# Kernel tuning notes

Measured on AMD Instinct MI355X. Metric: run time of the kernel, lower is better.

The kernel has to match this reference:

```python
import jax, jax.numpy as jnp
import numpy as np

N = 50000      # nodes
E = 800000     # edges
G = 512        # graphs
IN = 544; HID = 64; H = 4; OUT = 2
EPS = 1e-5

def setup_inputs():
    key = jax.random.key(0)
    ks = jax.random.split(key, 16)
    x = jax.random.normal(ks[0], (N, IN), jnp.float32)
    edge_index = jax.random.randint(ks[1], (2, E), 0, N, jnp.int64)
    batch = jnp.sort(jax.random.randint(ks[2], (N,), 0, G, jnp.int64))
    s = lambda k, shp, fan: jax.random.normal(k, shp, jnp.float32) / np.sqrt(fan)
    return {
        'x': x, 'edge_index': edge_index, 'batch': batch,
        'ln_g': jnp.ones((32,), jnp.float32), 'ln_b': jnp.zeros((32,), jnp.float32),
        'bn1_g': jnp.ones((512,), jnp.float32), 'bn1_b': jnp.zeros((512,), jnp.float32),
        'Wc': s(ks[3], (16, 512), 512), 'bc': jnp.zeros((16,), jnp.float32),
        'bn2_g': jnp.ones((48,), jnp.float32), 'bn2_b': jnp.zeros((48,), jnp.float32),
        'Wp': s(ks[4], (HID, 48), 48), 'bp': jnp.zeros((HID,), jnp.float32),
        'Wg': s(ks[5], (H * HID, HID), HID),
        'att_src': s(ks[6], (H, HID), HID), 'att_dst': s(ks[7], (H, HID), HID),
        'bg': jnp.zeros((H * HID,), jnp.float32),
        'bn3_g': jnp.ones((H * HID,), jnp.float32), 'bn3_b': jnp.zeros((H * HID,), jnp.float32),
        'W1': s(ks[8], (HID, H * HID), H * HID), 'b1': jnp.zeros((HID,), jnp.float32),
        'W2': s(ks[9], (OUT, HID), HID), 'b2': jnp.zeros((OUT,), jnp.float32),
    }

def _batchnorm(x, g, b):
    mu = jnp.mean(x, axis=0)
    var = jnp.var(x, axis=0)
    return (x - mu) * jax.lax.rsqrt(var + EPS) * g + b

def _forward(x, ln_g, ln_b, bn1_g, bn1_b, Wc, bc, bn2_g, bn2_b, Wp, bp,
             Wg, att_src, att_dst, bg, bn3_g, bn3_b, W1, b1, W2, b2,
             edge_index, batch):
    # feature split + norms
    x_cnn = _batchnorm(x[:, :512], bn1_g, bn1_b)
    f = x[:, 512:]
    mu = jnp.mean(f, axis=-1, keepdims=True)
    var = jnp.var(f, axis=-1, keepdims=True)
    f = (f - mu) * jax.lax.rsqrt(var + EPS) * ln_g + ln_b
    x_cnn = x_cnn @ Wc.T + bc                      # [N,16]
    z = jnp.concatenate([x_cnn, f], axis=1)        # [N,48]
    z = _batchnorm(z, bn2_g, bn2_b)
    z = jax.nn.relu(z @ Wp.T + bp)                 # [N,HID] (dropout=eval identity)
    # GATConv (concat=True, negative_slope=0.2)
    h = (z @ Wg.T).reshape(N, H, HID)              # [N,H,C]
    a_src = jnp.sum(h * att_src, axis=-1)          # [N,H]
    a_dst = jnp.sum(h * att_dst, axis=-1)          # [N,H]
    src, dst = edge_index[0], edge_index[1]
    e = jax.nn.leaky_relu(a_src[src] + a_dst[dst], 0.2)   # [E,H]
    m = jax.ops.segment_max(e, dst, num_segments=N)
    m = jnp.where(jnp.isfinite(m), m, 0.0)
    ex = jnp.exp(e - m[dst])
    s = jax.ops.segment_sum(ex, dst, num_segments=N)
    alpha = ex / jnp.maximum(s, 1e-16)[dst]               # [E,H]
    out = jax.ops.segment_sum(alpha[:, :, None] * h[src], dst, num_segments=N)
    out = out.reshape(N, H * HID) + bg
    # BatchNorm + ELU + mean pool + MLP head
    out = jax.nn.elu(_batchnorm(out, bn3_g, bn3_b))
    cnt = jax.ops.segment_sum(jnp.ones((N,), out.dtype), batch, num_segments=G)
    pooled = jax.ops.segment_sum(out, batch, num_segments=G) / jnp.maximum(cnt, 1.0)[:, None]
    hmlp = jax.nn.relu(pooled @ W1.T + b1)
    return hmlp @ W2.T + b2                        # [G,OUT]

def reference(x, edge_index, batch, ln_g, ln_b, bn1_g, bn1_b, Wc, bc, bn2_g, bn2_b,
              Wp, bp, Wg, att_src, att_dst, bg, bn3_g, bn3_b, W1, b1, W2, b2):
    return _forward(x, ln_g, ln_b, bn1_g, bn1_b, Wc, bc, bn2_g, bn2_b, Wp, bp,
                    Wg, att_src, att_dst, bg, bn3_g, bn3_b, W1, b1, W2, b2,
                    edge_index, batch)
```

## Files before the change

### kernel.cpp

```cpp
#include <hip/hip_runtime.h>

static constexpr int N_   = 50000;
static constexpr int E_   = 800000;
static constexpr int G_   = 512;
static constexpr int IN_  = 544;
static constexpr float EPS_ = 1e-5f;

static constexpr size_t OFF_BN1SUM = 0;
static constexpr size_t OFF_BN1SQ  = 2048;
static constexpr size_t OFF_BN2SUM = 4096;
static constexpr size_t OFF_BN2SQ  = 4288;
static constexpr size_t OFF_BN3SUM = 4480;
static constexpr size_t OFF_BN3SQ  = 5504;
static constexpr size_t OFF_COUNT  = 6528;
static constexpr size_t OFF_CUR    = 206528;
static constexpr size_t ZERO_BYTES = 406528;
static constexpr size_t OFF_OFFS   = 406528;
static constexpr size_t OFF_PART   = 606592;
static constexpr size_t OFF_WC2    = 606848;
static constexpr size_t OFF_C2     = 639616;
static constexpr size_t OFF_WP2    = 639744;
static constexpr size_t OFF_CP     = 652032;
static constexpr size_t OFF_WGT    = 652288;
static constexpr size_t OFF_ASRC   = 719872;
static constexpr size_t OFF_ADST   = 1519872;
static constexpr size_t OFF_SRCS   = 2319872;
static constexpr size_t OFF_Z      = 5519872;
static constexpr size_t OFF_H      = 15119872;
static constexpr size_t OFF_OUTP   = 66319872;
static constexpr size_t OFF_POOL   = 117519872;

#define DEV static __device__ __forceinline__

DEV float lrelu(float v) { return v > 0.f ? v : 0.2f * v; }
DEV unsigned short f2bf(float f) {
    unsigned u = __float_as_uint(f);
    return (unsigned short)((u + 0x7fffu + ((u >> 16) & 1u)) >> 16);
}

__global__ __launch_bounds__(512) void k_bn1_hist(
        const float* __restrict__ x, float* __restrict__ sum, float* __restrict__ sq,
        const int* __restrict__ ei, int* __restrict__ count) {
    __shared__ float4 ta[512];
    __shared__ float4 tb[512];
    int bid = blockIdx.x;
    int t = threadIdx.x;
    if (bid >= 256) {
        int k = (bid - 256) * 512 + t;
        if (k < E_) atomicAdd(&count[ei[E_ + k]], 1);
        return;
    }
    int cq = t & 127, rsub = t >> 7;
    int c4 = cq << 2;
    float4 a = make_float4(0.f, 0.f, 0.f, 0.f);
    float4 b = make_float4(0.f, 0.f, 0.f, 0.f);
    for (int r = bid * 4 + rsub; r < N_; r += 256 * 4) {
        float4 v = *(const float4*)(x + (size_t)r * IN_ + c4);
        a.x += v.x; a.y += v.y; a.z += v.z; a.w += v.w;
        b.x += v.x * v.x; b.y += v.y * v.y; b.z += v.z * v.z; b.w += v.w * v.w;
    }
    ta[t] = a; tb[t] = b;
    __syncthreads();
    if (t < 128) {
        float4 sa = ta[t], sb = tb[t];
#pragma unroll
        for (int r = 1; r < 4; r++) {
            float4 xa = ta[r * 128 + t], xb = tb[r * 128 + t];
            sa.x += xa.x; sa.y += xa.y; sa.z += xa.z; sa.w += xa.w;
            sb.x += xb.x; sb.y += xb.y; sb.z += xb.z; sb.w += xb.w;
        }
        int c = t << 2;
        atomicAdd(&sum[c + 0], sa.x); atomicAdd(&sum[c + 1], sa.y);
        atomicAdd(&sum[c + 2], sa.z); atomicAdd(&sum[c + 3], sa.w);
        atomicAdd(&sq[c + 0], sb.x);  atomicAdd(&sq[c + 1], sb.y);
        atomicAdd(&sq[c + 2], sb.z);  atomicAdd(&sq[c + 3], sb.w);
    }
}

__global__ __launch_bounds__(512) void k_fold1(
        const float* __restrict__ sum, const float* __restrict__ sq,
        const float* __restrict__ g, const float* __restrict__ b,
        const float* __restrict__ Wc, const float* __restrict__ bc,
        float* __restrict__ Wc2t, float* __restrict__ c2) {
    __shared__ float c2s[16];
    int j = threadIdx.x;
    if (j < 16) c2s[j] = 0.f;
    float mu  = sum[j] / (float)N_;
    float var = sq[j] / (float)N_ - mu * mu;
    float s   = g[j] * rsqrtf(var + EPS_);
    float tj  = b[j] - mu * s;
    __syncthreads();
    for (int i = 0; i < 16; i++) {
        float wv = Wc[i * 512 + j];
        Wc2t[i * 512 + j] = wv * s;
        float p = tj * wv;
        for (int m = 1; m < 64; m <<= 1) p += __shfl_xor(p, m);
        if ((j & 63) == 0) atomicAdd(&c2s[i], p);
    }
    __syncthreads();
    if (j < 16) c2[j] = c2s[j] + bc[j];
}

static constexpr int WSTRIDE = 516;
__global__ __launch_bounds__(512) void k_z(
        const float* __restrict__ x, const float* __restrict__ Wc2tg,
        const float* __restrict__ c2g, const float* __restrict__ lng,
        const float* __restrict__ lnb, float* __restrict__ z,
        float* __restrict__ bn2sum, float* __restrict__ bn2sq) {
    __shared__ float wc2[16 * WSTRIDE];
    __shared__ float c2s[16];
    __shared__ float bsum[48];
    __shared__ float bsq[48];
    int t = threadIdx.x;
    for (int q = t; q < 8192; q += 512) {
        int row = q >> 9, col = q & 511;
        wc2[row * WSTRIDE + col] = Wc2tg[q];
    }
    if (t < 16) c2s[t] = c2g[t];
    if (t < 48) { bsum[t] = 0.f; bsq[t] = 0.f; }
    __syncthreads();
    int nd = t >> 3, i = t & 7;
    int node = blockIdx.x * 64 + nd;
    bool valid = node < N_;
    int rn = valid ? node : N_ - 1;
    const float4* xr = (const float4*)(x + (size_t)rn * IN_);
    const float4* w0 = (const float4*)(wc2 + i * WSTRIDE);
    const float4* w1 = (const float4*)(wc2 + (i + 8) * WSTRIDE);
    float acc0 = c2s[i], acc1 = c2s[i + 8];
    for (int u = 0; u < 128; u++) {
        float4 xv = xr[u];
        float4 a4 = w0[u];
        float4 b4 = w1[u];
        acc0 += xv.x * a4.x + xv.y * a4.y + xv.z * a4.z + xv.w * a4.w;
        acc1 += xv.x * b4.x + xv.y * b4.y + xv.z * b4.z + xv.w * b4.w;
    }
    float v[4]; float sm = 0.f, sqv = 0.f;
#pragma unroll
    for (int jj = 0; jj < 4; jj++) {
        v[jj] = x[(size_t)rn * IN_ + 512 + i + 8 * jj];
        sm += v[jj]; sqv += v[jj] * v[jj];
    }
    for (int m = 1; m < 8; m <<= 1) {
        sm  += __shfl_xor(sm, m);
        sqv += __shfl_xor(sqv, m);
    }
    float mu  = sm * (1.f / 32.f);
    float var = sqv * (1.f / 32.f) - mu * mu;
    float rs  = rsqrtf(var + EPS_);
    float outc[6];
    outc[0] = acc0; outc[1] = acc1;
#pragma unroll
    for (int jj = 0; jj < 4; jj++) {
        int c = i + 8 * jj;
        outc[2 + jj] = (v[jj] - mu) * rs * lng[c] + lnb[c];
    }
    if (valid) {
        z[node * 48 + i]     = acc0;
        z[node * 48 + i + 8] = acc1;
#pragma unroll
        for (int jj = 0; jj < 4; jj++) z[node * 48 + 16 + i + 8 * jj] = outc[2 + jj];
    }
    float s6[6], q6[6];
#pragma unroll
    for (int k = 0; k < 6; k++) {
        float vv = valid ? outc[k] : 0.f;
        s6[k] = vv; q6[k] = vv * vv;
    }
#pragma unroll
    for (int m = 8; m < 64; m <<= 1) {
#pragma unroll
        for (int k = 0; k < 6; k++) {
            s6[k] += __shfl_xor(s6[k], m);
            q6[k] += __shfl_xor(q6[k], m);
        }
    }
    if ((t & 63) < 8) {
        int cols[6] = { i, i + 8, 16 + i, 24 + i, 32 + i, 40 + i };
#pragma unroll
        for (int k = 0; k < 6; k++) {
            atomicAdd(&bsum[cols[k]], s6[k]);
            atomicAdd(&bsq[cols[k]],  q6[k]);
        }
    }
    __syncthreads();
    if (t < 48) {
        atomicAdd(&bn2sum[t], bsum[t]);
        atomicAdd(&bn2sq[t],  bsq[t]);
    }
}

__global__ __launch_bounds__(256) void k_fold2_wgt(
        const float* __restrict__ sum, const float* __restrict__ sq,
        const float* __restrict__ g, const float* __restrict__ b,
        const float* __restrict__ Wp, const float* __restrict__ bp,
        float* __restrict__ Wp2, float* __restrict__ cp,
        const float* __restrict__ Wg, float* __restrict__ Wgt) {
    __shared__ float t2[48];
    int t = threadIdx.x;
    if (blockIdx.x > 0) {
        int idx = (blockIdx.x - 1) * 256 + t;
        int c = idx >> 6, k = idx & 63;
        Wgt[k * 256 + c] = Wg[idx];
        return;
    }
    if (t < 48) {
        float mu  = sum[t] / (float)N_;
        float var = sq[t] / (float)N_ - mu * mu;
        float s   = g[t] * rsqrtf(var + EPS_);
        t2[t] = b[t] - mu * s;
        for (int k = 0; k < 64; k++) Wp2[t * 64 + k] = Wp[k * 48 + t] * s;
    }
    __syncthreads();
    if (t < 64) {
        float acc = bp[t];
        for (int j = 0; j < 48; j++) acc += t2[j] * Wp[t * 48 + j];
        cp[t] = acc;
    }
}

__global__ void k_scan1(const int* __restrict__ count, int* __restrict__ offs,
                        int* __restrict__ part) {
    __shared__ int sd[1024];
    int t = threadIdx.x;
    int idx = blockIdx.x * 1024 + t;
    int v = (idx < N_) ? count[idx] : 0;
    sd[t] = v;
    for (int off = 1; off < 1024; off <<= 1) {
        __syncthreads();
        int tmp = (t >= off) ? sd[t - off] : 0;
        __syncthreads();
        sd[t] += tmp;
    }
    if (idx < N_) offs[idx] = sd[t] - v;
    if (t == 1023) part[blockIdx.x] = sd[1023];
}
__global__ void k_scan23(int* __restrict__ offs, const int* __restrict__ part) {
    __shared__ int bs;
    int t = threadIdx.x, b = blockIdx.x;
    if (t < 64) {
        int v = (t < b) ? part[t] : 0;
        for (int m = 1; m < 64; m <<= 1) v += __shfl_xor(v, m);
        if (t == 0) bs = v;
    }
    __syncthreads();
    int idx = b * 1024 + t;
    if (idx < N_) offs[idx] += bs;
}

__global__ void k_scatter(const int* __restrict__ ei, const int* __restrict__ offs,
                          int* __restrict__ cur, int* __restrict__ srcsort) {
    int k = blockIdx.x * 256 + threadIdx.x;
    int src = ei[k], dst = ei[E_ + k];
    int pos = offs[dst] + atomicAdd(&cur[dst], 1);
    srcsort[pos] = src;
}

__global__ __launch_bounds__(512) void k_h2(
        const float* __restrict__ z, const float* __restrict__ Wp2g,
        const float* __restrict__ cpg, const float* __restrict__ Wgtg,
        const float* __restrict__ att_s, const float* __restrict__ att_d,
        ushort4* __restrict__ hbf, float* __restrict__ asrc, float* __restrict__ adst) {
    __shared__ float4 wgh[32 * 64];
    __shared__ float  z1t[128 * 64];
    __shared__ float  wp2[48 * 64];
    __shared__ float  cps[64];
    __shared__ float4 ats[64];
    __shared__ float4 atd[64];
    int t = threadIdx.x;
    int base = blockIdx.x * 128;
    {
        const float4* z4 = (const float4*)(z + (size_t)base * 48);
        float4* zt4 = (float4*)wgh;
        for (int q = t; q < 1536; q += 512) zt4[q] = z4[q];
    }
    for (int q = t; q < 3072; q += 512) wp2[q] = Wp2g[q];
    if (t < 64) {
        cps[t] = cpg[t];
        ats[t] = ((const float4*)att_s)[t];
        atd[t] = ((const float4*)att_d)[t];
    }
    __syncthreads();
    int w = t >> 6, l = t & 63;
    {
        float wpr[48];
#pragma unroll
        for (int j = 0; j < 48; j++) wpr[j] = wp2[j * 64 + l];
        const float* zt = (const float*)wgh;
        for (int p = 0; p < 16; p++) {
            int nd = p * 8 + w;
            float acc = cps[l];
            const float* zr = zt + nd * 48;
#pragma unroll
            for (int j = 0; j < 48; j++) acc += zr[j] * wpr[j];
            z1t[nd * 64 + l] = fmaxf(acc, 0.f);
        }
    }
    const float4* wg4 = (const float4*)Wgtg;
    float4 acc[16];
#pragma unroll
    for (int nd = 0; nd < 16; nd++) acc[nd] = make_float4(0.f, 0.f, 0.f, 0.f);
    for (int half = 0; half < 2; half++) {
        __syncthreads();
        for (int q = t; q < 2048; q += 512) wgh[q] = wg4[half * 2048 + q];
        __syncthreads();
        int kbase = half * 32;
        for (int kk = 0; kk < 32; kk++) {
            float4 wv = wgh[kk * 64 + l];
            int k = kbase + kk;
#pragma unroll
            for (int nd = 0; nd < 16; nd++) {
                float zv = z1t[(w * 16 + nd) * 64 + k];
                acc[nd].x += zv * wv.x; acc[nd].y += zv * wv.y;
                acc[nd].z += zv * wv.z; acc[nd].w += zv * wv.w;
            }
        }
    }
    float4 as4 = ats[l], ad4 = atd[l];
#pragma unroll
    for (int nd = 0; nd < 16; nd++) {
        int node = base + w * 16 + nd;
        if (node < N_) {
            ushort4 hv;
            hv.x = f2bf(acc[nd].x); hv.y = f2bf(acc[nd].y);
            hv.z = f2bf(acc[nd].z); hv.w = f2bf(acc[nd].w);
            hbf[(size_t)node * 64 + l] = hv;
            float pa = acc[nd].x * as4.x + acc[nd].y * as4.y +
                       acc[nd].z * as4.z + acc[nd].w * as4.w;
            float pb = acc[nd].x * ad4.x + acc[nd].y * ad4.y +
                       acc[nd].z * ad4.z + acc[nd].w * ad4.w;
            for (int m = 1; m < 16; m <<= 1) {
                pa += __shfl_xor(pa, m);
                pb += __shfl_xor(pb, m);
            }
            if ((l & 15) == 0) {
                asrc[node * 4 + (l >> 4)] = pa;
                adst[node * 4 + (l >> 4)] = pb;
            }
        }
    }
}

__global__ __launch_bounds__(256) void k_agg(
        const int* __restrict__ count, const int* __restrict__ offs,
        const int* __restrict__ srcsort, const float* __restrict__ asrc,
        const float* __restrict__ adst, const ushort4* __restrict__ hbf,
        const float* __restrict__ bg, float* __restrict__ outpre) {
    __shared__ int   s_src[4][128];
    __shared__ float s_wf[4][512];
    int w = threadIdx.x >> 6, l = threadIdx.x & 63;
    int dst = blockIdx.x * 4 + w;
    const float4* asrc4 = (const float4*)asrc;
    float4* out4 = (float4*)outpre;
    float4 bgv = ((const float4*)bg)[l];
    int deg = count[dst];
    if (deg == 0) { out4[dst * 64 + l] = bgv; return; }
    int base = offs[dst];
    float4 ad = ((const float4*)adst)[dst];
    const float NEGINF = -__builtin_inff();
    float4 e0 = make_float4(NEGINF, NEGINF, NEGINF, NEGINF);
    float4 e1 = make_float4(NEGINF, NEGINF, NEGINF, NEGINF);
    if (l < deg) {
        int s0 = srcsort[base + l];
        s_src[w][l] = s0;
        float4 a = asrc4[s0];
        e0 = make_float4(lrelu(a.x + ad.x), lrelu(a.y + ad.y),
                         lrelu(a.z + ad.z), lrelu(a.w + ad.w));
    }
    if (l + 64 < deg) {
        int s1 = srcsort[base + l + 64];
        s_src[w][l + 64] = s1;
        float4 a = asrc4[s1];
        e1 = make_float4(lrelu(a.x + ad.x), lrelu(a.y + ad.y),
                         lrelu(a.z + ad.z), lrelu(a.w + ad.w));
    }
    float4 mx = make_float4(fmaxf(e0.x, e1.x), fmaxf(e0.y, e1.y),
                            fmaxf(e0.z, e1.z), fmaxf(e0.w, e1.w));
    for (int j = l + 128; j < deg; j += 64) {
        int s2 = srcsort[base + j];
        float4 a = asrc4[s2];
        mx.x = fmaxf(mx.x, lrelu(a.x + ad.x)); mx.y = fmaxf(mx.y, lrelu(a.y + ad.y));
        mx.z = fmaxf(mx.z, lrelu(a.z + ad.z)); mx.w = fmaxf(mx.w, lrelu(a.w + ad.w));
    }
    for (int m = 1; m < 64; m <<= 1) {
        mx.x = fmaxf(mx.x, __shfl_xor(mx.x, m));
        mx.y = fmaxf(mx.y, __shfl_xor(mx.y, m));
        mx.z = fmaxf(mx.z, __shfl_xor(mx.z, m));
        mx.w = fmaxf(mx.w, __shfl_xor(mx.w, m));
    }
    float4 sv = make_float4(0.f, 0.f, 0.f, 0.f);
    if (l < deg) {
        float4 ex = make_float4(__expf(e0.x - mx.x), __expf(e0.y - mx.y),
                                __expf(e0.z - mx.z), __expf(e0.w - mx.w));
        *(float4*)&s_wf[w][l * 4] = ex;
        sv.x += ex.x; sv.y += ex.y; sv.z += ex.z; sv.w += ex.w;
    }
    if (l + 64 < deg) {
        float4 ex = make_float4(__expf(e1.x - mx.x), __expf(e1.y - mx.y),
                                __expf(e1.z - mx.z), __expf(e1.w - mx.w));
        *(float4*)&s_wf[w][(l + 64) * 4] = ex;
        sv.x += ex.x; sv.y += ex.y; sv.z += ex.z; sv.w += ex.w;
    }
    for (int j = l + 128; j < deg; j += 64) {
        int s2 = srcsort[base + j];
        float4 a = asrc4[s2];
        sv.x += __expf(lrelu(a.x + ad.x) - mx.x);
        sv.y += __expf(lrelu(a.y + ad.y) - mx.y);
        sv.z += __expf(lrelu(a.z + ad.z) - mx.z);
        sv.w += __expf(lrelu(a.w + ad.w) - mx.w);
    }
    for (int m = 1; m < 64; m <<= 1) {
        sv.x += __shfl_xor(sv.x, m); sv.y += __shfl_xor(sv.y, m);
        sv.z += __shfl_xor(sv.z, m); sv.w += __shfl_xor(sv.w, m);
    }
    int hd = l >> 4;
    float mh  = hd == 0 ? mx.x : hd == 1 ? mx.y : hd == 2 ? mx.z : mx.w;
    float sh  = hd == 0 ? sv.x : hd == 1 ? sv.y : hd == 2 ? sv.z : sv.w;
    float adh = hd == 0 ? ad.x : hd == 1 ? ad.y : hd == 2 ? ad.z : ad.w;
    float inv = 1.f / fmaxf(sh, 1e-16f);
    float4 accv = make_float4(0.f, 0.f, 0.f, 0.f);
    const uint2* h2p = (const uint2*)hbf;
    int dcap = deg < 128 ? deg : 128;
#pragma unroll 2
    for (int j = 0; j < dcap; j++) {
        int src = s_src[w][j];
        float wgt = s_wf[w][j * 4 + hd] * inv;
        uint2 u = h2p[(size_t)src * 64 + l];
        accv.x += wgt * __uint_as_float(u.x << 16);
        accv.y += wgt * __uint_as_float(u.x & 0xffff0000u);
        accv.z += wgt * __uint_as_float(u.y << 16);
        accv.w += wgt * __uint_as_float(u.y & 0xffff0000u);
    }
    for (int j = 128; j < deg; j++) {
        int src = srcsort[base + j];
        float4 a = asrc4[src];
        float ah = hd == 0 ? a.x : hd == 1 ? a.y : hd == 2 ? a.z : a.w;
        float wgt = __expf(lrelu(ah + adh) - mh) * inv;
        uint2 u = h2p[(size_t)src * 64 + l];
        accv.x += wgt * __uint_as_float(u.x << 16);
        accv.y += wgt * __uint_as_float(u.x & 0xffff0000u);
        accv.z += wgt * __uint_as_float(u.y << 16);
        accv.w += wgt * __uint_as_float(u.y & 0xffff0000u);
    }
    out4[dst * 64 + l] = make_float4(accv.x + bgv.x, accv.y + bgv.y,
                                     accv.z + bgv.z, accv.w + bgv.w);
}

__global__ __launch_bounds__(256) void k_bn3_stats(
        const float* __restrict__ op, float* __restrict__ sum, float* __restrict__ sq) {
    __shared__ float4 ta[256];
    __shared__ float4 tb[256];
    int t = threadIdx.x;
    int cq = t & 63, rsub = t >> 6;
    int c4 = cq << 2;
    float4 a = make_float4(0.f, 0.f, 0.f, 0.f);
    float4 b = make_float4(0.f, 0.f, 0.f, 0.f);
    for (int r = blockIdx.x * 4 + rsub; r < N_; r += gridDim.x * 4) {
        float4 v = *(const float4*)(op + (size_t)r * 256 + c4);
        a.x += v.x; a.y += v.y; a.z += v.z; a.w += v.w;
        b.x += v.x * v.x; b.y += v.y * v.y; b.z += v.z * v.z; b.w += v.w * v.w;
    }
    ta[t] = a; tb[t] = b;
    __syncthreads();
    if (t < 64) {
        float4 sa = ta[t], sb = tb[t];
#pragma unroll
        for (int r = 1; r < 4; r++) {
            float4 xa = ta[r * 64 + t], xb = tb[r * 64 + t];
            sa.x += xa.x; sa.y += xa.y; sa.z += xa.z; sa.w += xa.w;
            sb.x += xb.x; sb.y += xb.y; sb.z += xb.z; sb.w += xb.w;
        }
        int c = t << 2;
        atomicAdd(&sum[c + 0], sa.x); atomicAdd(&sum[c + 1], sa.y);
        atomicAdd(&sum[c + 2], sa.z); atomicAdd(&sum[c + 3], sa.w);
        atomicAdd(&sq[c + 0], sb.x);  atomicAdd(&sq[c + 1], sb.y);
        atomicAdd(&sq[c + 2], sb.z);  atomicAdd(&sq[c + 3], sb.w);
    }
}

__global__ __launch_bounds__(256) void k_pool_mlp(
        const float* __restrict__ op, const int* __restrict__ batch,
        const float* __restrict__ bn3sum, const float* __restrict__ bn3sq,
        const float* __restrict__ bn3g, const float* __restrict__ bn3b,
        const float* __restrict__ W1, const float* __restrict__ b1,
        const float* __restrict__ W2, const float* __restrict__ b2,
        float* __restrict__ out) {
    __shared__ float4 tile[256];
    __shared__ float  pl[256];
    __shared__ float  hm[64];
    int g = blockIdx.x;
    int t = threadIdx.x;
    int cq = t & 63, rsub = t >> 6;
    int c4 = cq << 2;
    int lo = 0, hi = N_;
    while (lo < hi) { int mid = (lo + hi) >> 1; if (batch[mid] < g) lo = mid + 1; else hi = mid; }
    int start = lo;
    hi = N_;
    while (lo < hi) { int mid = (lo + hi) >> 1; if (batch[mid] < g + 1) lo = mid + 1; else hi = mid; }
    int end = lo;
    float scv[4], shv[4];
#pragma unroll
    for (int k = 0; k < 4; k++) {
        int c = c4 + k;
        float mu  = bn3sum[c] / (float)N_;
        float var = bn3sq[c] / (float)N_ - mu * mu;
        float s   = bn3g[c] * rsqrtf(var + EPS_);
        scv[k] = s; shv[k] = bn3b[c] - mu * s;
    }
    float4 acc = make_float4(0.f, 0.f, 0.f, 0.f);
    for (int n = start + rsub; n < end; n += 4) {
        float4 v = *(const float4*)(op + (size_t)n * 256 + c4);
        float e0 = v.x * scv[0] + shv[0], e1 = v.y * scv[1] + shv[1];
        float e2 = v.z * scv[2] + shv[2], e3 = v.w * scv[3] + shv[3];
        acc.x += (e0 > 0.f) ? e0 : expm1f(e0);
        acc.y += (e1 > 0.f) ? e1 : expm1f(e1);
        acc.z += (e2 > 0.f) ? e2 : expm1f(e2);
        acc.w += (e3 > 0.f) ? e3 : expm1f(e3);
    }
    tile[t] = acc;
    __syncthreads();
    if (t < 64) {
        float4 s = tile[t];
#pragma unroll
        for (int r = 1; r < 4; r++) {
            float4 xv = tile[r * 64 + t];
            s.x += xv.x; s.y += xv.y; s.z += xv.z; s.w += xv.w;
        }
        float icn = 1.f / fmaxf((float)(end - start), 1.f);
        ((float4*)pl)[t] = make_float4(s.x * icn, s.y * icn, s.z * icn, s.w * icn);
    }
    __syncthreads();
    {
        int j = t >> 2, part = t & 3;
        const float* w1r = W1 + j * 256 + part * 64;
        const float* plr = pl + part * 64;
        float a = 0.f;
#pragma unroll
        for (int c = 0; c < 64; c++) a += w1r[c] * plr[c];
        a += __shfl_xor(a, 1);
        a += __shfl_xor(a, 2);
        if (part == 0) hm[j] = fmaxf(a + b1[j], 0.f);
    }
    __syncthreads();
    if (t < 128) {
        int j = t >> 6, k = t & 63;
        float p = W2[j * 64 + k] * hm[k];
        for (int m = 1; m < 64; m <<= 1) p += __shfl_xor(p, m);
        if (k == 0) out[g * 2 + j] = p + b2[j];
    }
}

extern "C" void kernel_launch(void* const* d_in, const int* in_sizes, int n_in,
                              void* d_out, int out_size, void* d_ws, size_t ws_size,
                              hipStream_t stream) {
    const float* x    = (const float*)d_in[0];
    const int*   ei   = (const int*)d_in[1];
    const int*   batch= (const int*)d_in[2];
    const float* lng  = (const float*)d_in[3];
    const float* lnb  = (const float*)d_in[4];
    const float* bn1g = (const float*)d_in[5];
    const float* bn1b = (const float*)d_in[6];
    const float* Wc   = (const float*)d_in[7];
    const float* bc   = (const float*)d_in[8];
    const float* bn2g = (const float*)d_in[9];
    const float* bn2b = (const float*)d_in[10];
    const float* Wp   = (const float*)d_in[11];
    const float* bp   = (const float*)d_in[12];
    const float* Wg   = (const float*)d_in[13];
    const float* atts = (const float*)d_in[14];
    const float* attd = (const float*)d_in[15];
    const float* bg   = (const float*)d_in[16];
    const float* bn3g = (const float*)d_in[17];
    const float* bn3b = (const float*)d_in[18];
    const float* W1   = (const float*)d_in[19];
    const float* b1   = (const float*)d_in[20];
    const float* W2   = (const float*)d_in[21];
    const float* b2   = (const float*)d_in[22];
    float* out = (float*)d_out;

    char* w8 = (char*)d_ws;
    float* bn1sum = (float*)(w8 + OFF_BN1SUM);
    float* bn1sq  = (float*)(w8 + OFF_BN1SQ);
    float* bn2sum = (float*)(w8 + OFF_BN2SUM);
    float* bn2sq  = (float*)(w8 + OFF_BN2SQ);
    float* bn3sum = (float*)(w8 + OFF_BN3SUM);
    float* bn3sq  = (float*)(w8 + OFF_BN3SQ);
    int*   count  = (int*)(w8 + OFF_COUNT);
    int*   cur    = (int*)(w8 + OFF_CUR);
    int*   offs   = (int*)(w8 + OFF_OFFS);
    int*   part   = (int*)(w8 + OFF_PART);
    float* Wc2t   = (float*)(w8 + OFF_WC2);
    float* c2     = (float*)(w8 + OFF_C2);
    float* Wp2    = (float*)(w8 + OFF_WP2);
    float* cp     = (float*)(w8 + OFF_CP);
    float* Wgt    = (float*)(w8 + OFF_WGT);
    float* asrc   = (float*)(w8 + OFF_ASRC);
    float* adst   = (float*)(w8 + OFF_ADST);
    int*   srcs   = (int*)(w8 + OFF_SRCS);
    float* z      = (float*)(w8 + OFF_Z);
    ushort4* hbf  = (ushort4*)(w8 + OFF_H);
    float* outp   = (float*)(w8 + OFF_OUTP);

    hipMemsetAsync(d_ws, 0, ZERO_BYTES, stream);

    const int HISTB = (E_ + 511) / 512;
    k_bn1_hist<<<256 + HISTB, 512, 0, stream>>>(x, bn1sum, bn1sq, ei, count);
    k_fold1<<<1, 512, 0, stream>>>(bn1sum, bn1sq, bn1g, bn1b, Wc, bc, Wc2t, c2);
    k_z<<<(N_ + 63) / 64, 512, 0, stream>>>(x, Wc2t, c2, lng, lnb, z, bn2sum, bn2sq);
    const int SCANB = (N_ + 1023) / 1024;
    k_scan1<<<SCANB, 1024, 0, stream>>>(count, offs, part);
    k_scan23<<<SCANB, 1024, 0, stream>>>(offs, part);
    k_fold2_wgt<<<65, 256, 0, stream>>>(bn2sum, bn2sq, bn2g, bn2b, Wp, bp, Wp2, cp, Wg, Wgt);
    k_scatter<<<E_ / 256, 256, 0, stream>>>(ei, offs, cur, srcs);
    k_h2<<<(N_ + 127) / 128, 512, 0, stream>>>(z, Wp2, cp, Wgt, atts, attd, hbf, asrc, adst);
    k_agg<<<N_ / 4, 256, 0, stream>>>(count, offs, srcs, asrc, adst, hbf, bg, outp);
    k_bn3_stats<<<256, 256, 0, stream>>>(outp, bn3sum, bn3sq);
    k_pool_mlp<<<G_, 256, 0, stream>>>(outp, batch, bn3sum, bn3sq, bn3g, bn3b,
                                       W1, b1, W2, b2, out);
}
```

Measured before the change: 555.0 us.

## Store GAT output in bf16, tile k_z over node pairs, vectorize k_h2 loops

The aggregation output is now stored as bf16 instead of fp32, which halves the bytes written by k_agg and read by the bn3 stats and pooling kernels. The edge histogram is merged into the grid-stride loop of the bn1 stats kernel, which now runs with a fixed 2048x256 grid. k_z computes two nodes per thread so each weight read from shared memory is reused, and k_h2 uses float4 loads from shared memory in both of its inner products. k_bn3_stats also gets more blocks. Rounding to bf16 adds error to the BN3 statistics and to the pooled values.

```diff
diff --git a/kernel.cpp b/kernel.cpp
--- a/kernel.cpp
+++ b/kernel.cpp
@@ -28,7 +28,6 @@
 static constexpr size_t OFF_Z      = 5519872;
 static constexpr size_t OFF_H      = 15119872;
 static constexpr size_t OFF_OUTP   = 66319872;
-static constexpr size_t OFF_POOL   = 117519872;
 
 #define DEV static __device__ __forceinline__
 
@@ -38,23 +37,17 @@
     return (unsigned short)((u + 0x7fffu + ((u >> 16) & 1u)) >> 16);
 }
 
-__global__ __launch_bounds__(512) void k_bn1_hist(
+__global__ __launch_bounds__(256) void k_bn1_hist(
         const float* __restrict__ x, float* __restrict__ sum, float* __restrict__ sq,
         const int* __restrict__ ei, int* __restrict__ count) {
-    __shared__ float4 ta[512];
-    __shared__ float4 tb[512];
-    int bid = blockIdx.x;
+    __shared__ float4 ta[256];
+    __shared__ float4 tb[256];
     int t = threadIdx.x;
-    if (bid >= 256) {
-        int k = (bid - 256) * 512 + t;
-        if (k < E_) atomicAdd(&count[ei[E_ + k]], 1);
-        return;
-    }
     int cq = t & 127, rsub = t >> 7;
     int c4 = cq << 2;
     float4 a = make_float4(0.f, 0.f, 0.f, 0.f);
     float4 b = make_float4(0.f, 0.f, 0.f, 0.f);
-    for (int r = bid * 4 + rsub; r < N_; r += 256 * 4) {
+    for (int r = blockIdx.x * 2 + rsub; r < N_; r += gridDim.x * 2) {
         float4 v = *(const float4*)(x + (size_t)r * IN_ + c4);
         a.x += v.x; a.y += v.y; a.z += v.z; a.w += v.w;
         b.x += v.x * v.x; b.y += v.y * v.y; b.z += v.z * v.z; b.w += v.w * v.w;
@@ -63,18 +56,17 @@
     __syncthreads();
     if (t < 128) {
         float4 sa = ta[t], sb = tb[t];
-#pragma unroll
-        for (int r = 1; r < 4; r++) {
-            float4 xa = ta[r * 128 + t], xb = tb[r * 128 + t];
-            sa.x += xa.x; sa.y += xa.y; sa.z += xa.z; sa.w += xa.w;
-            sb.x += xb.x; sb.y += xb.y; sb.z += xb.z; sb.w += xb.w;
-        }
+        float4 xa = ta[128 + t], xb = tb[128 + t];
+        sa.x += xa.x; sa.y += xa.y; sa.z += xa.z; sa.w += xa.w;
+        sb.x += xb.x; sb.y += xb.y; sb.z += xb.z; sb.w += xb.w;
         int c = t << 2;
         atomicAdd(&sum[c + 0], sa.x); atomicAdd(&sum[c + 1], sa.y);
         atomicAdd(&sum[c + 2], sa.z); atomicAdd(&sum[c + 3], sa.w);
         atomicAdd(&sq[c + 0], sb.x);  atomicAdd(&sq[c + 1], sb.y);
         atomicAdd(&sq[c + 2], sb.z);  atomicAdd(&sq[c + 3], sb.w);
     }
+    for (int k = blockIdx.x * 256 + t; k < E_; k += gridDim.x * 256)
+        atomicAdd(&count[ei[E_ + k]], 1);
 }
 
 __global__ __launch_bounds__(512) void k_fold1(
@@ -119,52 +111,63 @@
     if (t < 16) c2s[t] = c2g[t];
     if (t < 48) { bsum[t] = 0.f; bsq[t] = 0.f; }
     __syncthreads();
-    int nd = t >> 3, i = t & 7;
-    int node = blockIdx.x * 64 + nd;
-    bool valid = node < N_;
-    int rn = valid ? node : N_ - 1;
-    const float4* xr = (const float4*)(x + (size_t)rn * IN_);
+    int pr = t >> 3, i = t & 7;
+    int n0 = blockIdx.x * 128 + pr * 2;
+    int n1 = n0 + 1;
+    bool v0 = n0 < N_, v1 = n1 < N_;
+    const float4* xr0 = (const float4*)(x + (size_t)(v0 ? n0 : N_ - 1) * IN_);
+    const float4* xr1 = (const float4*)(x + (size_t)(v1 ? n1 : N_ - 1) * IN_);
     const float4* w0 = (const float4*)(wc2 + i * WSTRIDE);
     const float4* w1 = (const float4*)(wc2 + (i + 8) * WSTRIDE);
-    float acc0 = c2s[i], acc1 = c2s[i + 8];
+    float a00 = c2s[i], a01 = c2s[i + 8];
+    float a10 = a00, a11 = a01;
     for (int u = 0; u < 128; u++) {
-        float4 xv = xr[u];
-        float4 a4 = w0[u];
-        float4 b4 = w1[u];
-        acc0 += xv.x * a4.x + xv.y * a4.y + xv.z * a4.z + xv.w * a4.w;
-        acc1 += xv.x * b4.x + xv.y * b4.y + xv.z * b4.z + xv.w * b4.w;
-    }
-    float v[4]; float sm = 0.f, sqv = 0.f;
+        float4 xa = xr0[u], xb = xr1[u];
+        float4 p = w0[u], q4 = w1[u];
+        a00 += xa.x * p.x + xa.y * p.y + xa.z * p.z + xa.w * p.w;
+        a01 += xa.x * q4.x + xa.y * q4.y + xa.z * q4.z + xa.w * q4.w;
+        a10 += xb.x * p.x + xb.y * p.y + xb.z * p.z + xb.w * p.w;
+        a11 += xb.x * q4.x + xb.y * q4.y + xb.z * q4.z + xb.w * q4.w;
+    }
+    float va[4], vb[4];
+    float sm0 = 0.f, sq0 = 0.f, sm1 = 0.f, sq1 = 0.f;
 #pragma unroll
     for (int jj = 0; jj < 4; jj++) {
-        v[jj] = x[(size_t)rn * IN_ + 512 + i + 8 * jj];
-        sm += v[jj]; sqv += v[jj] * v[jj];
+        va[jj] = x[(size_t)(v0 ? n0 : N_ - 1) * IN_ + 512 + i + 8 * jj];
+        vb[jj] = x[(size_t)(v1 ? n1 : N_ - 1) * IN_ + 512 + i + 8 * jj];
+        sm0 += va[jj]; sq0 += va[jj] * va[jj];
+        sm1 += vb[jj]; sq1 += vb[jj] * vb[jj];
     }
     for (int m = 1; m < 8; m <<= 1) {
-        sm  += __shfl_xor(sm, m);
-        sqv += __shfl_xor(sqv, m);
-    }
-    float mu  = sm * (1.f / 32.f);
-    float var = sqv * (1.f / 32.f) - mu * mu;
-    float rs  = rsqrtf(var + EPS_);
-    float outc[6];
-    outc[0] = acc0; outc[1] = acc1;
+        sm0 += __shfl_xor(sm0, m); sq0 += __shfl_xor(sq0, m);
+        sm1 += __shfl_xor(sm1, m); sq1 += __shfl_xor(sq1, m);
+    }
+    float mu0 = sm0 * (1.f / 32.f), rs0 = rsqrtf(sq0 * (1.f / 32.f) - mu0 * mu0 + EPS_);
+    float mu1 = sm1 * (1.f / 32.f), rs1 = rsqrtf(sq1 * (1.f / 32.f) - mu1 * mu1 + EPS_);
+    float outa[6], outb[6];
+    outa[0] = a00; outa[1] = a01; outb[0] = a10; outb[1] = a11;
 #pragma unroll
     for (int jj = 0; jj < 4; jj++) {
         int c = i + 8 * jj;
-        outc[2 + jj] = (v[jj] - mu) * rs * lng[c] + lnb[c];
-    }
-    if (valid) {
-        z[node * 48 + i]     = acc0;
-        z[node * 48 + i + 8] = acc1;
-#pragma unroll
-        for (int jj = 0; jj < 4; jj++) z[node * 48 + 16 + i + 8 * jj] = outc[2 + jj];
+        float gg = lng[c], bb = lnb[c];
+        outa[2 + jj] = (va[jj] - mu0) * rs0 * gg + bb;
+        outb[2 + jj] = (vb[jj] - mu1) * rs1 * gg + bb;
+    }
+    int cols[6] = { i, i + 8, 16 + i, 24 + i, 32 + i, 40 + i };
+    if (v0) {
+#pragma unroll
+        for (int k = 0; k < 6; k++) z[n0 * 48 + cols[k]] = outa[k];
+    }
+    if (v1) {
+#pragma unroll
+        for (int k = 0; k < 6; k++) z[n1 * 48 + cols[k]] = outb[k];
     }
     float s6[6], q6[6];
 #pragma unroll
     for (int k = 0; k < 6; k++) {
-        float vv = valid ? outc[k] : 0.f;
-        s6[k] = vv; q6[k] = vv * vv;
+        float pa = v0 ? outa[k] : 0.f;
+        float pb = v1 ? outb[k] : 0.f;
+        s6[k] = pa + pb; q6[k] = pa * pa + pb * pb;
     }
 #pragma unroll
     for (int m = 8; m < 64; m <<= 1) {
@@ -175,7 +178,6 @@
         }
     }
     if ((t & 63) < 8) {
-        int cols[6] = { i, i + 8, 16 + i, 24 + i, 32 + i, 40 + i };
 #pragma unroll
         for (int k = 0; k < 6; k++) {
             atomicAdd(&bsum[cols[k]], s6[k]);
@@ -260,9 +262,9 @@
         const float* __restrict__ cpg, const float* __restrict__ Wgtg,
         const float* __restrict__ att_s, const float* __restrict__ att_d,
         ushort4* __restrict__ hbf, float* __restrict__ asrc, float* __restrict__ adst) {
-    __shared__ float4 wgh[32 * 64];
-    __shared__ float  z1t[128 * 64];
-    __shared__ float  wp2[48 * 64];
+    __shared__ __align__(16) float4 wgh[32 * 64];
+    __shared__ __align__(16) float  z1t[128 * 64];
+    __shared__ __align__(16) float  wp2[48 * 64];
     __shared__ float  cps[64];
     __shared__ float4 ats[64];
     __shared__ float4 atd[64];
@@ -289,9 +291,13 @@
         for (int p = 0; p < 16; p++) {
             int nd = p * 8 + w;
             float acc = cps[l];
-            const float* zr = zt + nd * 48;
-#pragma unroll
-            for (int j = 0; j < 48; j++) acc += zr[j] * wpr[j];
+            const float4* zr4 = (const float4*)(zt + nd * 48);
+#pragma unroll
+            for (int u = 0; u < 12; u++) {
+                float4 zv = zr4[u];
+                acc += zv.x * wpr[u * 4 + 0] + zv.y * wpr[u * 4 + 1] +
+                       zv.z * wpr[u * 4 + 2] + zv.w * wpr[u * 4 + 3];
+            }
             z1t[nd * 64 + l] = fmaxf(acc, 0.f);
         }
     }
@@ -304,14 +310,18 @@
         for (int q = t; q < 2048; q += 512) wgh[q] = wg4[half * 2048 + q];
         __syncthreads();
         int kbase = half * 32;
-        for (int kk = 0; kk < 32; kk++) {
-            float4 wv = wgh[kk * 64 + l];
-            int k = kbase + kk;
+        for (int k4 = 0; k4 < 8; k4++) {
+            float4 wv0 = wgh[(k4 * 4 + 0) * 64 + l];
+            float4 wv1 = wgh[(k4 * 4 + 1) * 64 + l];
+            float4 wv2 = wgh[(k4 * 4 + 2) * 64 + l];
+            float4 wv3 = wgh[(k4 * 4 + 3) * 64 + l];
 #pragma unroll
             for (int nd = 0; nd < 16; nd++) {
-                float zv = z1t[(w * 16 + nd) * 64 + k];
-                acc[nd].x += zv * wv.x; acc[nd].y += zv * wv.y;
-                acc[nd].z += zv * wv.z; acc[nd].w += zv * wv.w;
+                float4 zv = *(const float4*)&z1t[(w * 16 + nd) * 64 + kbase + k4 * 4];
+                acc[nd].x += zv.x * wv0.x + zv.y * wv1.x + zv.z * wv2.x + zv.w * wv3.x;
+                acc[nd].y += zv.x * wv0.y + zv.y * wv1.y + zv.z * wv2.y + zv.w * wv3.y;
+                acc[nd].z += zv.x * wv0.z + zv.y * wv1.z + zv.z * wv2.z + zv.w * wv3.z;
+                acc[nd].w += zv.x * wv0.w + zv.y * wv1.w + zv.z * wv2.w + zv.w * wv3.w;
             }
         }
     }
@@ -344,16 +354,20 @@
         const int* __restrict__ count, const int* __restrict__ offs,
         const int* __restrict__ srcsort, const float* __restrict__ asrc,
         const float* __restrict__ adst, const ushort4* __restrict__ hbf,
-        const float* __restrict__ bg, float* __restrict__ outpre) {
+        const float* __restrict__ bg, ushort4* __restrict__ outbf) {
     __shared__ int   s_src[4][128];
     __shared__ float s_wf[4][512];
     int w = threadIdx.x >> 6, l = threadIdx.x & 63;
     int dst = blockIdx.x * 4 + w;
     const float4* asrc4 = (const float4*)asrc;
-    float4* out4 = (float4*)outpre;
     float4 bgv = ((const float4*)bg)[l];
     int deg = count[dst];
-    if (deg == 0) { out4[dst * 64 + l] = bgv; return; }
+    if (deg == 0) {
+        ushort4 o;
+        o.x = f2bf(bgv.x); o.y = f2bf(bgv.y); o.z = f2bf(bgv.z); o.w = f2bf(bgv.w);
+        outbf[(size_t)dst * 64 + l] = o;
+        return;
+    }
     int base = offs[dst];
     float4 ad = ((const float4*)adst)[dst];
     const float NEGINF = -__builtin_inff();
@@ -441,23 +455,28 @@
         accv.z += wgt * __uint_as_float(u.y << 16);
         accv.w += wgt * __uint_as_float(u.y & 0xffff0000u);
     }
-    out4[dst * 64 + l] = make_float4(accv.x + bgv.x, accv.y + bgv.y,
-                                     accv.z + bgv.z, accv.w + bgv.w);
+    ushort4 o;
+    o.x = f2bf(accv.x + bgv.x); o.y = f2bf(accv.y + bgv.y);
+    o.z = f2bf(accv.z + bgv.z); o.w = f2bf(accv.w + bgv.w);
+    outbf[(size_t)dst * 64 + l] = o;
 }
 
 __global__ __launch_bounds__(256) void k_bn3_stats(
-        const float* __restrict__ op, float* __restrict__ sum, float* __restrict__ sq) {
+        const uint2* __restrict__ op2, float* __restrict__ sum, float* __restrict__ sq) {
     __shared__ float4 ta[256];
     __shared__ float4 tb[256];
     int t = threadIdx.x;
     int cq = t & 63, rsub = t >> 6;
-    int c4 = cq << 2;
     float4 a = make_float4(0.f, 0.f, 0.f, 0.f);
     float4 b = make_float4(0.f, 0.f, 0.f, 0.f);
     for (int r = blockIdx.x * 4 + rsub; r < N_; r += gridDim.x * 4) {
-        float4 v = *(const float4*)(op + (size_t)r * 256 + c4);
-        a.x += v.x; a.y += v.y; a.z += v.z; a.w += v.w;
-        b.x += v.x * v.x; b.y += v.y * v.y; b.z += v.z * v.z; b.w += v.w * v.w;
+        uint2 u = op2[(size_t)r * 64 + cq];
+        float x0 = __uint_as_float(u.x << 16);
+        float x1 = __uint_as_float(u.x & 0xffff0000u);
+        float x2 = __uint_as_float(u.y << 16);
+        float x3 = __uint_as_float(u.y & 0xffff0000u);
+        a.x += x0; a.y += x1; a.z += x2; a.w += x3;
+        b.x += x0 * x0; b.y += x1 * x1; b.z += x2 * x2; b.w += x3 * x3;
     }
     ta[t] = a; tb[t] = b;
     __syncthreads();
@@ -478,7 +497,7 @@
 }
 
 __global__ __launch_bounds__(256) void k_pool_mlp(
-        const float* __restrict__ op, const int* __restrict__ batch,
+        const uint2* __restrict__ op2, const int* __restrict__ batch,
         const float* __restrict__ bn3sum, const float* __restrict__ bn3sq,
         const float* __restrict__ bn3g, const float* __restrict__ bn3b,
         const float* __restrict__ W1, const float* __restrict__ b1,
@@ -508,9 +527,11 @@
     }
     float4 acc = make_float4(0.f, 0.f, 0.f, 0.f);
     for (int n = start + rsub; n < end; n += 4) {
-        float4 v = *(const float4*)(op + (size_t)n * 256 + c4);
-        float e0 = v.x * scv[0] + shv[0], e1 = v.y * scv[1] + shv[1];
-        float e2 = v.z * scv[2] + shv[2], e3 = v.w * scv[3] + shv[3];
+        uint2 u = op2[(size_t)n * 64 + cq];
+        float e0 = __uint_as_float(u.x << 16)          * scv[0] + shv[0];
+        float e1 = __uint_as_float(u.x & 0xffff0000u)  * scv[1] + shv[1];
+        float e2 = __uint_as_float(u.y << 16)          * scv[2] + shv[2];
+        float e3 = __uint_as_float(u.y & 0xffff0000u)  * scv[3] + shv[3];
         acc.x += (e0 > 0.f) ? e0 : expm1f(e0);
         acc.y += (e1 > 0.f) ? e1 : expm1f(e1);
         acc.z += (e2 > 0.f) ? e2 : expm1f(e2);
@@ -598,14 +619,13 @@
     int*   srcs   = (int*)(w8 + OFF_SRCS);
     float* z      = (float*)(w8 + OFF_Z);
     ushort4* hbf  = (ushort4*)(w8 + OFF_H);
-    float* outp   = (float*)(w8 + OFF_OUTP);
+    ushort4* outp = (ushort4*)(w8 + OFF_OUTP);
 
     hipMemsetAsync(d_ws, 0, ZERO_BYTES, stream);
 
-    const int HISTB = (E_ + 511) / 512;
-    k_bn1_hist<<<256 + HISTB, 512, 0, stream>>>(x, bn1sum, bn1sq, ei, count);
+    k_bn1_hist<<<2048, 256, 0, stream>>>(x, bn1sum, bn1sq, ei, count);
     k_fold1<<<1, 512, 0, stream>>>(bn1sum, bn1sq, bn1g, bn1b, Wc, bc, Wc2t, c2);
-    k_z<<<(N_ + 63) / 64, 512, 0, stream>>>(x, Wc2t, c2, lng, lnb, z, bn2sum, bn2sq);
+    k_z<<<(N_ + 127) / 128, 512, 0, stream>>>(x, Wc2t, c2, lng, lnb, z, bn2sum, bn2sq);
     const int SCANB = (N_ + 1023) / 1024;
     k_scan1<<<SCANB, 1024, 0, stream>>>(count, offs, part);
     k_scan23<<<SCANB, 1024, 0, stream>>>(offs, part);
@@ -613,7 +633,7 @@
     k_scatter<<<E_ / 256, 256, 0, stream>>>(ei, offs, cur, srcs);
     k_h2<<<(N_ + 127) / 128, 512, 0, stream>>>(z, Wp2, cp, Wgt, atts, attd, hbf, asrc, adst);
     k_agg<<<N_ / 4, 256, 0, stream>>>(count, offs, srcs, asrc, adst, hbf, bg, outp);
-    k_bn3_stats<<<256, 256, 0, stream>>>(outp, bn3sum, bn3sq);
-    k_pool_mlp<<<G_, 256, 0, stream>>>(outp, batch, bn3sum, bn3sq, bn3g, bn3b,
-                                       W1, b1, W2, b2, out);
-}
+    k_bn3_stats<<<1024, 256, 0, stream>>>((const uint2*)outp, bn3sum, bn3sq);
+    k_pool_mlp<<<G_, 256, 0, stream>>>((const uint2*)outp, batch, bn3sum, bn3sq,
+                                       bn3g, bn3b, W1, b1, W2, b2, out);
+}
```

After: 793.3 us. +43.0%, slower.
